# Performance work log

Measured on AMD Instinct MI355X. Metric: run time of the kernel, lower is better.

Reference implementation:

```python
import math
import jax, jax.numpy as jnp
import numpy as np

L = 16
LOG2T = 19
T = 1 << LOG2T
F = 2
N_MIN = 16
N_MAX = 2048
N_PTS = 1048576

# intended geometric growth factor (source has a parenthesization bug)
_B = math.exp((math.log(N_MAX) - math.log(N_MIN)) / (L - 1))
RESOLUTIONS = [int(math.floor(N_MIN * (_B ** i))) for i in range(L)]

# 8 corner offsets of a voxel, [8, 3]
_OFFS_NP = np.stack(np.meshgrid([0, 1], [0, 1], [0, 1], indexing='ij'), -1).reshape(8, 3)
# spatial hash primes from Instant-NGP
_PRIMES_NP = np.array([1, 2654435761, 805459861], dtype=np.uint32)


def setup_inputs() -> dict:
    key = jax.random.key(0)
    k1, k2 = jax.random.split(key)
    x = jax.random.uniform(k1, (N_PTS, 3), dtype=jnp.float32)  # positions in [0,1)
    table = jax.random.normal(k2, (L, T, F), dtype=jnp.float32) * 1e-4
    return {"x": x, "table": table}


def _encode(x, table):
    offs_i = jnp.asarray(_OFFS_NP, dtype=jnp.uint32)          # [8,3]
    offs_f = jnp.asarray(_OFFS_NP, dtype=x.dtype)             # [8,3]
    primes = jnp.asarray(_PRIMES_NP)                          # [3] uint32
    mask = jnp.uint32(T - 1)
    outs = []
    for lvl in range(L):
        res = RESOLUTIONS[lvl]
        xs = x * res                                           # [N,3]
        x0 = jnp.floor(xs)
        w = xs - x0                                            # [N,3] trilerp weights
        # corner integer coords, [N,8,3]
        c = x0.astype(jnp.uint32)[:, None, :] + offs_i[None]
        # spatial hash: xor of coord*prime, masked to T (T is a power of 2)
        hp = c * primes                                        # uint32 wraparound mul
        h = (hp[..., 0] ^ hp[..., 1] ^ hp[..., 2]) & mask      # [N,8]
        feats = table[lvl][h.astype(jnp.int32)]                # [N,8,F] gather
        # trilinear weights: prod over dims of (w if corner==1 else 1-w)
        wts = jnp.prod(jnp.where(offs_f[None] == 1.0, w[:, None, :], 1.0 - w[:, None, :]), axis=-1)  # [N,8]
        outs.append(jnp.einsum('nc,ncf->nf', wts, feats))      # [N,F]
    return jnp.concatenate(outs, axis=-1)                      # [N, L*F]


def reference(x, table):
    return _encode(x, table)
```

## Files before the change

kernel.cpp:

```cpp
#include <hip/hip_runtime.h>
#include <cmath>

#define NPTS   1048576
#define NLVL   16
#define TMASK  ((1u << 19) - 1u)
#define P1     2654435761u
#define P2     805459861u

typedef float v2f __attribute__((ext_vector_type(2)));
typedef float v4f __attribute__((ext_vector_type(4)));

__global__ __launch_bounds__(256) void hashgrid_lvl(
    const float* __restrict__ x,
    const float* __restrict__ tb,
    float* __restrict__ wsl,
    float rf,
    int ostride)
{
    const int n = blockIdx.x * 256 + threadIdx.x;

    const float px = __builtin_nontemporal_load(x + 3 * (size_t)n + 0);
    const float py = __builtin_nontemporal_load(x + 3 * (size_t)n + 1);
    const float pz = __builtin_nontemporal_load(x + 3 * (size_t)n + 2);

    const float xs0 = px * rf, xs1 = py * rf, xs2 = pz * rf;
    const float f0 = floorf(xs0), f1 = floorf(xs1), f2 = floorf(xs2);
    const float w0 = xs0 - f0, w1 = xs1 - f1, w2 = xs2 - f2;

    const uint32_t i0 = (uint32_t)f0;
    const uint32_t i1 = (uint32_t)f1;
    const uint32_t i2 = (uint32_t)f2;

    const uint32_t A0 = i0,      A1 = i0 + 1u;
    const uint32_t B0 = i1 * P1, B1 = B0 + P1;
    const uint32_t C0 = i2 * P2, C1 = C0 + P2;

    const uint32_t h000 = (A0 ^ B0 ^ C0) & TMASK;
    const uint32_t h001 = (A0 ^ B0 ^ C1) & TMASK;
    const uint32_t h010 = (A0 ^ B1 ^ C0) & TMASK;
    const uint32_t h011 = (A0 ^ B1 ^ C1) & TMASK;
    const uint32_t h100 = (A1 ^ B0 ^ C0) & TMASK;
    const uint32_t h101 = (A1 ^ B0 ^ C1) & TMASK;
    const uint32_t h110 = (A1 ^ B1 ^ C0) & TMASK;
    const uint32_t h111 = (A1 ^ B1 ^ C1) & TMASK;

    const float2 g000 = *(const float2*)(tb + 2 * (size_t)h000);
    const float2 g001 = *(const float2*)(tb + 2 * (size_t)h001);
    const float2 g010 = *(const float2*)(tb + 2 * (size_t)h010);
    const float2 g011 = *(const float2*)(tb + 2 * (size_t)h011);
    const float2 g100 = *(const float2*)(tb + 2 * (size_t)h100);
    const float2 g101 = *(const float2*)(tb + 2 * (size_t)h101);
    const float2 g110 = *(const float2*)(tb + 2 * (size_t)h110);
    const float2 g111 = *(const float2*)(tb + 2 * (size_t)h111);

    const float u0 = 1.0f - w0, u1 = 1.0f - w1, u2 = 1.0f - w2;
    const float wt000 = (u0 * u1) * u2;
    const float wt001 = (u0 * u1) * w2;
    const float wt010 = (u0 * w1) * u2;
    const float wt011 = (u0 * w1) * w2;
    const float wt100 = (w0 * u1) * u2;
    const float wt101 = (w0 * u1) * w2;
    const float wt110 = (w0 * w1) * u2;
    const float wt111 = (w0 * w1) * w2;

    float a0 = wt000 * g000.x;
    float a1 = wt000 * g000.y;
    a0 += wt001 * g001.x;  a1 += wt001 * g001.y;
    a0 += wt010 * g010.x;  a1 += wt010 * g010.y;
    a0 += wt011 * g011.x;  a1 += wt011 * g011.y;
    a0 += wt100 * g100.x;  a1 += wt100 * g100.y;
    a0 += wt101 * g101.x;  a1 += wt101 * g101.y;
    a0 += wt110 * g110.x;  a1 += wt110 * g110.y;
    a0 += wt111 * g111.x;  a1 += wt111 * g111.y;

    if (ostride == 2) {
        v2f r; r.x = a0; r.y = a1;
        __builtin_nontemporal_store(r, (v2f*)(wsl + (size_t)n * 2));
    } else {
        wsl[(size_t)n * 32 + 0] = a0;
        wsl[(size_t)n * 32 + 1] = a1;
    }
}

__global__ __launch_bounds__(256) void hashgrid_transpose(
    const float* __restrict__ ws,
    float* __restrict__ out)
{
    const int n = blockIdx.x * 256 + threadIdx.x;
    float acc[2 * NLVL];
#pragma unroll
    for (int l = 0; l < NLVL; ++l) {
        const v2f g = __builtin_nontemporal_load(
            (const v2f*)(ws + ((size_t)l << 21) + (size_t)n * 2));
        acc[2 * l + 0] = g.x;
        acc[2 * l + 1] = g.y;
    }
    v4f* op = (v4f*)(out + (size_t)n * 32);
#pragma unroll
    for (int k = 0; k < 8; ++k) {
        v4f v; v.x = acc[4*k]; v.y = acc[4*k+1]; v.z = acc[4*k+2]; v.w = acc[4*k+3];
        op[k] = v;
    }
}

extern "C" void kernel_launch(void* const* d_in, const int* in_sizes, int n_in,
                              void* d_out, int out_size, void* d_ws, size_t ws_size,
                              hipStream_t stream) {
    const float* x     = (const float*)d_in[0];
    const float* table = (const float*)d_in[1];
    float* out         = (float*)d_out;
    float* ws          = (float*)d_ws;

    double (*volatile p_log)(double)          = log;
    double (*volatile p_exp)(double)          = exp;
    double (*volatile p_pow)(double, double)  = pow;
    double (*volatile p_floor)(double)        = floor;

    const double b = p_exp((p_log(2048.0) - p_log(16.0)) / 15.0);

    const bool use_ws = ws_size >= (size_t)NLVL * NPTS * 2 * sizeof(float);

    for (int l = 0; l < NLVL; ++l) {
        const int res = (int)p_floor(16.0 * p_pow(b, (double)l));
        if (use_ws) {
            hashgrid_lvl<<<NPTS / 256, 256, 0, stream>>>(
                x, table + ((size_t)l << 20), ws + ((size_t)l << 21),
                (float)res, 2);
        } else {
            hashgrid_lvl<<<NPTS / 256, 256, 0, stream>>>(
                x, table + ((size_t)l << 20), out + 2 * l,
                (float)res, 32);
        }
    }
    if (use_ws) {
        hashgrid_transpose<<<NPTS / 256, 256, 0, stream>>>(ws, out);
    }
}
```

Baseline: 571.6 us.

## Split high-level table gathers into two hash-range passes for cache locality

For levels above 4, the per-level kernel now runs twice, and each pass gathers only the corners whose hash falls in one half of the table. The second pass adds its result to the partial sum left by the first. The aim is to keep each pass's working set (half of a 4 MB level table) resident in L2/MALL so the random gathers hit cache more often. The cost is recomputing positions and hashes twice per point and an extra read and write of the workspace for those levels.

```diff
diff --git a/kernel.cpp b/kernel.cpp
--- a/kernel.cpp
+++ b/kernel.cpp
@@ -3,83 +3,79 @@
 
 #define NPTS   1048576
 #define NLVL   16
-#define TMASK  ((1u << 19) - 1u)
+#define T      (1u << 19)
+#define TMASK  (T - 1u)
 #define P1     2654435761u
 #define P2     805459861u
 
 typedef float v2f __attribute__((ext_vector_type(2)));
 typedef float v4f __attribute__((ext_vector_type(4)));
 
-__global__ __launch_bounds__(256) void hashgrid_lvl(
+#define PREAMBLE                                                             \
+    const int n = blockIdx.x * 256 + threadIdx.x;                            \
+    const float px = __builtin_nontemporal_load(x + 3 * (size_t)n + 0);      \
+    const float py = __builtin_nontemporal_load(x + 3 * (size_t)n + 1);      \
+    const float pz = __builtin_nontemporal_load(x + 3 * (size_t)n + 2);      \
+    const float xs0 = px * rf, xs1 = py * rf, xs2 = pz * rf;                 \
+    const float f0 = floorf(xs0), f1 = floorf(xs1), f2 = floorf(xs2);        \
+    const float w0 = xs0 - f0, w1 = xs1 - f1, w2 = xs2 - f2;                 \
+    const uint32_t i0 = (uint32_t)f0;                                        \
+    const uint32_t i1 = (uint32_t)f1;                                        \
+    const uint32_t i2 = (uint32_t)f2;                                        \
+    const uint32_t A0 = i0,      A1 = i0 + 1u;                               \
+    const uint32_t B0 = i1 * P1, B1 = B0 + P1;                               \
+    const uint32_t C0 = i2 * P2, C1 = C0 + P2;                               \
+    const uint32_t h[8] = {                                                  \
+        (A0 ^ B0 ^ C0) & TMASK, (A0 ^ B0 ^ C1) & TMASK,                      \
+        (A0 ^ B1 ^ C0) & TMASK, (A0 ^ B1 ^ C1) & TMASK,                      \
+        (A1 ^ B0 ^ C0) & TMASK, (A1 ^ B0 ^ C1) & TMASK,                      \
+        (A1 ^ B1 ^ C0) & TMASK, (A1 ^ B1 ^ C1) & TMASK };                    \
+    const float u0 = 1.0f - w0, u1 = 1.0f - w1, u2 = 1.0f - w2;              \
+    const float wt[8] = {                                                    \
+        (u0 * u1) * u2, (u0 * u1) * w2, (u0 * w1) * u2, (u0 * w1) * w2,      \
+        (w0 * u1) * u2, (w0 * u1) * w2, (w0 * w1) * u2, (w0 * w1) * w2 };
+
+__global__ __launch_bounds__(256) void hashgrid_lvl1(
+    const float* __restrict__ x,
+    const float* __restrict__ tb,
+    float* __restrict__ wsl,
+    float rf)
+{
+    PREAMBLE
+    float a0 = 0.f, a1 = 0.f;
+#pragma unroll
+    for (int c = 0; c < 8; ++c) {
+        const float2 g = *(const float2*)(tb + 2 * (size_t)h[c]);
+        a0 += wt[c] * g.x;
+        a1 += wt[c] * g.y;
+    }
+    v2f r; r.x = a0; r.y = a1;
+    __builtin_nontemporal_store(r, (v2f*)(wsl + (size_t)n * 2));
+}
+
+__global__ __launch_bounds__(256) void hashgrid_lvl_range(
     const float* __restrict__ x,
     const float* __restrict__ tb,
     float* __restrict__ wsl,
     float rf,
-    int ostride)
+    uint32_t lo, uint32_t hi, int addin)
 {
-    const int n = blockIdx.x * 256 + threadIdx.x;
-
-    const float px = __builtin_nontemporal_load(x + 3 * (size_t)n + 0);
-    const float py = __builtin_nontemporal_load(x + 3 * (size_t)n + 1);
-    const float pz = __builtin_nontemporal_load(x + 3 * (size_t)n + 2);
-
-    const float xs0 = px * rf, xs1 = py * rf, xs2 = pz * rf;
-    const float f0 = floorf(xs0), f1 = floorf(xs1), f2 = floorf(xs2);
-    const float w0 = xs0 - f0, w1 = xs1 - f1, w2 = xs2 - f2;
-
-    const uint32_t i0 = (uint32_t)f0;
-    const uint32_t i1 = (uint32_t)f1;
-    const uint32_t i2 = (uint32_t)f2;
-
-    const uint32_t A0 = i0,      A1 = i0 + 1u;
-    const uint32_t B0 = i1 * P1, B1 = B0 + P1;
-    const uint32_t C0 = i2 * P2, C1 = C0 + P2;
-
-    const uint32_t h000 = (A0 ^ B0 ^ C0) & TMASK;
-    const uint32_t h001 = (A0 ^ B0 ^ C1) & TMASK;
-    const uint32_t h010 = (A0 ^ B1 ^ C0) & TMASK;
-    const uint32_t h011 = (A0 ^ B1 ^ C1) & TMASK;
-    const uint32_t h100 = (A1 ^ B0 ^ C0) & TMASK;
-    const uint32_t h101 = (A1 ^ B0 ^ C1) & TMASK;
-    const uint32_t h110 = (A1 ^ B1 ^ C0) & TMASK;
-    const uint32_t h111 = (A1 ^ B1 ^ C1) & TMASK;
-
-    const float2 g000 = *(const float2*)(tb + 2 * (size_t)h000);
-    const float2 g001 = *(const float2*)(tb + 2 * (size_t)h001);
-    const float2 g010 = *(const float2*)(tb + 2 * (size_t)h010);
-    const float2 g011 = *(const float2*)(tb + 2 * (size_t)h011);
-    const float2 g100 = *(const float2*)(tb + 2 * (size_t)h100);
-    const float2 g101 = *(const float2*)(tb + 2 * (size_t)h101);
-    const float2 g110 = *(const float2*)(tb + 2 * (size_t)h110);
-    const float2 g111 = *(const float2*)(tb + 2 * (size_t)h111);
-
-    const float u0 = 1.0f - w0, u1 = 1.0f - w1, u2 = 1.0f - w2;
-    const float wt000 = (u0 * u1) * u2;
-    const float wt001 = (u0 * u1) * w2;
-    const float wt010 = (u0 * w1) * u2;
-    const float wt011 = (u0 * w1) * w2;
-    const float wt100 = (w0 * u1) * u2;
-    const float wt101 = (w0 * u1) * w2;
-    const float wt110 = (w0 * w1) * u2;
-    const float wt111 = (w0 * w1) * w2;
-
-    float a0 = wt000 * g000.x;
-    float a1 = wt000 * g000.y;
-    a0 += wt001 * g001.x;  a1 += wt001 * g001.y;
-    a0 += wt010 * g010.x;  a1 += wt010 * g010.y;
-    a0 += wt011 * g011.x;  a1 += wt011 * g011.y;
-    a0 += wt100 * g100.x;  a1 += wt100 * g100.y;
-    a0 += wt101 * g101.x;  a1 += wt101 * g101.y;
-    a0 += wt110 * g110.x;  a1 += wt110 * g110.y;
-    a0 += wt111 * g111.x;  a1 += wt111 * g111.y;
-
-    if (ostride == 2) {
-        v2f r; r.x = a0; r.y = a1;
-        __builtin_nontemporal_store(r, (v2f*)(wsl + (size_t)n * 2));
-    } else {
-        wsl[(size_t)n * 32 + 0] = a0;
-        wsl[(size_t)n * 32 + 1] = a1;
+    PREAMBLE
+    float a0 = 0.f, a1 = 0.f;
+    if (addin) {
+        const v2f p = __builtin_nontemporal_load((const v2f*)(wsl + (size_t)n * 2));
+        a0 = p.x; a1 = p.y;
     }
+#pragma unroll
+    for (int c = 0; c < 8; ++c) {
+        if (h[c] >= lo && h[c] < hi) {
+            const float2 g = *(const float2*)(tb + 2 * (size_t)h[c]);
+            a0 += wt[c] * g.x;
+            a1 += wt[c] * g.y;
+        }
+    }
+    v2f r; r.x = a0; r.y = a1;
+    __builtin_nontemporal_store(r, (v2f*)(wsl + (size_t)n * 2));
 }
 
 __global__ __launch_bounds__(256) void hashgrid_transpose(
@@ -103,6 +99,24 @@
     }
 }
 
+__global__ __launch_bounds__(256) void hashgrid_lvl_direct(
+    const float* __restrict__ x,
+    const float* __restrict__ tb,
+    float* __restrict__ outl,
+    float rf)
+{
+    PREAMBLE
+    float a0 = 0.f, a1 = 0.f;
+#pragma unroll
+    for (int c = 0; c < 8; ++c) {
+        const float2 g = *(const float2*)(tb + 2 * (size_t)h[c]);
+        a0 += wt[c] * g.x;
+        a1 += wt[c] * g.y;
+    }
+    outl[(size_t)n * 32 + 0] = a0;
+    outl[(size_t)n * 32 + 1] = a1;
+}
+
 extern "C" void kernel_launch(void* const* d_in, const int* in_sizes, int n_in,
                               void* d_out, int out_size, void* d_ws, size_t ws_size,
                               hipStream_t stream) {
@@ -119,20 +133,26 @@
     const double b = p_exp((p_log(2048.0) - p_log(16.0)) / 15.0);
 
     const bool use_ws = ws_size >= (size_t)NLVL * NPTS * 2 * sizeof(float);
+    const int grid = NPTS / 256;
 
     for (int l = 0; l < NLVL; ++l) {
         const int res = (int)p_floor(16.0 * p_pow(b, (double)l));
-        if (use_ws) {
-            hashgrid_lvl<<<NPTS / 256, 256, 0, stream>>>(
-                x, table + ((size_t)l << 20), ws + ((size_t)l << 21),
-                (float)res, 2);
+        const float rf = (float)res;
+        const float* tb = table + ((size_t)l << 20);
+
+        if (!use_ws) {
+            hashgrid_lvl_direct<<<grid, 256, 0, stream>>>(x, tb, out + 2 * l, rf);
+            continue;
+        }
+        float* wsl = ws + ((size_t)l << 21);
+        if (l <= 4) {
+            hashgrid_lvl1<<<grid, 256, 0, stream>>>(x, tb, wsl, rf);
         } else {
-            hashgrid_lvl<<<NPTS / 256, 256, 0, stream>>>(
-                x, table + ((size_t)l << 20), out + 2 * l,
-                (float)res, 32);
+            hashgrid_lvl_range<<<grid, 256, 0, stream>>>(x, tb, wsl, rf, 0u,    T/2, 0);
+            hashgrid_lvl_range<<<grid, 256, 0, stream>>>(x, tb, wsl, rf, T/2,  T,   1);
         }
     }
     if (use_ws) {
-        hashgrid_transpose<<<NPTS / 256, 256, 0, stream>>>(ws, out);
+        hashgrid_transpose<<<grid, 256, 0, stream>>>(ws, out);
     }
 }
```

Measured after the change: 686.1 us. 1.2x slower.
